# Performance work log

Measured on AMD Instinct MI355X. Metric: run time of the kernel, lower is better.

## Reference

```python
import jax, jax.numpy as jnp
import numpy as np

B, N, H = 8192, 8, 256
EDGE_DIM = 16
HALF = EDGE_DIM // 2  # 8: emb half + scalar half
THR = 0.4
PAIR_OFFS = [(0, N), (0, 2 * N), (N, 2 * N)]  # (text,audio), (text,facial), (audio,facial)
E_PER = 6 * (N - 1) + 6 * N  # 90 edges per sample


def _base_edge_index():
    # Static per-sample topology (matches the torch loop ordering exactly).
    src, dst = [], []
    for m in range(3):  # temporal edges, both directions interleaved
        for i in range(N - 1):
            u, v = m * N + i, m * N + i + 1
            src += [u, v]; dst += [v, u]
    for oa, ob in PAIR_OFFS:  # cross-modal edges
        for i in range(N):
            src += [oa + i, ob + i]; dst += [ob + i, oa + i]
    return np.array([src, dst], dtype=np.int64)  # (2, E_PER)

_BASE_EI = _base_edge_index()


def _l2norm(x):
    return x / jnp.maximum(jnp.linalg.norm(x, axis=-1, keepdims=True), 1e-12)


def setup_inputs() -> dict:
    key = jax.random.key(0)
    ks = jax.random.split(key, 6)
    s = 1.0 / np.sqrt(H)
    return {
        "z_text_segs": jax.random.normal(ks[0], (B, N, H), jnp.float32),
        "z_audio_segs": jax.random.normal(ks[1], (B, N, H), jnp.float32),
        "z_facial_segs": jax.random.normal(ks[2], (B, N, H), jnp.float32),
        "Wq": jax.random.normal(ks[3], (H // 2, H), jnp.float32) * s,
        "bq": jnp.zeros((H // 2,), jnp.float32),
        "Wk": jax.random.normal(ks[4], (H // 2, H), jnp.float32) * s,
        "bk": jnp.zeros((H // 2,), jnp.float32),
        "emb": jax.random.normal(ks[5], (5, HALF), jnp.float32),
    }


def reference(z_text_segs, z_audio_segs, z_facial_segs, Wq, bq, Wk, bk, emb):
    nodes = jnp.concatenate([z_text_segs, z_audio_segs, z_facial_segs], axis=1)  # (B, 3N, H)
    q = _l2norm(nodes @ Wq.T + bq)  # (B, 3N, H/2)
    k = _l2norm(nodes @ Wk.T + bk)

    # Cross-modal discrepancy, pair-major then segment (matches loop order): P = 3N
    a_idx = np.concatenate([oa + np.arange(N) for oa, _ in PAIR_OFFS])
    b_idx = np.concatenate([ob + np.arange(N) for _, ob in PAIR_OFFS])
    disc = 1.0 - jax.nn.sigmoid(jnp.einsum('bph,bph->bp', q[:, a_idx], k[:, b_idx]))  # (B, P)

    etype = jnp.where(disc > THR, 4, 3)  # (B, P) int
    z = jnp.zeros_like(disc)
    # scalar half: [disc_w, temp_dist, direction, etype/4, pad...]
    cross_scal = jnp.stack([disc, z, z, etype.astype(jnp.float32) / 4.0] + [z] * (HALF - 4), axis=-1)
    cross_attr = jnp.concatenate([emb[etype], cross_scal], axis=-1)  # (B, P, EDGE_DIM)
    cross_attr = jnp.repeat(cross_attr, 2, axis=1)  # both directions share the attr

    # Temporal edge attrs: constant per modality m in {0,1,2}
    mz = jnp.zeros((3,), jnp.float32)
    t_scal = jnp.stack([mz, jnp.full((3,), 1.0 / N), jnp.ones((3,)),
                        jnp.arange(3, dtype=jnp.float32) / 4.0] + [mz] * (HALF - 4), axis=-1)
    t_attr = jnp.concatenate([emb[:3], t_scal], axis=-1)  # (3, EDGE_DIM)
    t_attr = jnp.repeat(t_attr, 2 * (N - 1), axis=0)  # (6(N-1), EDGE_DIM)
    t_attr = jnp.broadcast_to(t_attr, (B,) + t_attr.shape)

    edge_attr = jnp.concatenate([t_attr, cross_attr], axis=1).reshape(B * E_PER, EDGE_DIM)

    ei = _BASE_EI[:, None, :] + (np.arange(B, dtype=np.int64) * 3 * N)[None, :, None]
    edge_index = jnp.asarray(ei.reshape(2, B * E_PER))

    node_feats = nodes.reshape(B * 3 * N, H)
    batch_vec = jnp.repeat(jnp.arange(B), 3 * N)
    return node_feats, edge_index, edge_attr, batch_vec
```

## Files before the change

### kernel.cpp

```cpp
#include <hip/hip_runtime.h>
#include <stdint.h>

#define BB 8192
#define HH 256
#define HO 128
#define NODES 24
#define EPER 90
#define NF_SIZE (BB * NODES * HH)
#define EI_OFF  NF_SIZE
#define EI_SIZE (2 * BB * EPER)
#define EA_OFF  (EI_OFF + EI_SIZE)
#define EA_SIZE (BB * EPER * 16)
#define BV_OFF  (EA_OFF + EA_SIZE)

typedef float f4 __attribute__((ext_vector_type(4)));

#define SL(dst, base, IMM) \
    asm volatile("s_load_dwordx4 %0, %1, " IMM : "=s"(dst) : "s"(base))

#define SWAIT8(a0,a1,a2,a3,a4,a5,a6,a7) \
    asm volatile("s_waitcnt lgkmcnt(0)" \
                 : "+s"(a0),"+s"(a1),"+s"(a2),"+s"(a3), \
                   "+s"(a4),"+s"(a5),"+s"(a6),"+s"(a7))

#define FMA4(acc, W_, X_) \
    acc = fmaf((W_)[0],(X_)[0],acc); acc = fmaf((W_)[1],(X_)[1],acc); \
    acc = fmaf((W_)[2],(X_)[2],acc); acc = fmaf((W_)[3],(X_)[3],acc);

#define LD8(BUF, ADDR) \
    SL(BUF##0, ADDR, "0x0");    SL(BUF##1, ADDR, "0x400"); \
    SL(BUF##2, ADDR, "0x800");  SL(BUF##3, ADDR, "0xc00"); \
    SL(BUF##4, ADDR, "0x1000"); SL(BUF##5, ADDR, "0x1400"); \
    SL(BUF##6, ADDR, "0x1800"); SL(BUF##7, ADDR, "0x1c00");

#define C8(ACC0, ACC1, BUF) \
    FMA4(ACC0[0], w0, BUF##0) FMA4(ACC1[0], w1, BUF##0) \
    FMA4(ACC0[1], w0, BUF##1) FMA4(ACC1[1], w1, BUF##1) \
    FMA4(ACC0[2], w0, BUF##2) FMA4(ACC1[2], w1, BUF##2) \
    FMA4(ACC0[3], w0, BUF##3) FMA4(ACC1[3], w1, BUF##3) \
    FMA4(ACC0[4], w0, BUF##4) FMA4(ACC1[4], w1, BUF##4) \
    FMA4(ACC0[5], w0, BUF##5) FMA4(ACC1[5], w1, BUF##5) \
    FMA4(ACC0[6], w0, BUF##6) FMA4(ACC1[6], w1, BUF##6) \
    FMA4(ACC0[7], w0, BUF##7) FMA4(ACC1[7], w1, BUF##7)

__global__ __launch_bounds__(256) void transpose_w(
    const float4* __restrict__ Wq4, const float4* __restrict__ Wk4,
    float4* __restrict__ ws)
{
    int idx = blockIdx.x * 256 + threadIdx.x;
    const float4* src = (idx < 8192) ? Wq4 : Wk4;
    int j  = idx & 8191;
    int o  = j >> 6;
    int kk = j & 63;
    float4 v = src[j];
    ws[(idx & 8192) + kk * 128 + o] = v;
}

__global__ __launch_bounds__(256) void htdg_kernel(
    const float* __restrict__ zt, const float* __restrict__ za,
    const float* __restrict__ zf,
    const float* __restrict__ bq, const float* __restrict__ bk,
    const float* __restrict__ emb, const float* __restrict__ wt,
    float* __restrict__ out)
{
    __shared__ float uv[2 * 32 * HO];
    __shared__ float nrm_part[2][256];
    __shared__ float dot_part[2][192];
    __shared__ float rnorm_s[2][32];
    __shared__ float disc_s[2][24];
    __shared__ int   et_s[2][24];
    __shared__ float emb_s[40];

    const int b0  = blockIdx.x * 2;
    const int tid = threadIdx.x;

    {
        const f4* zt4 = (const f4*)zt + (size_t)b0 * 512;
        const f4* za4 = (const f4*)za + (size_t)b0 * 512;
        const f4* zf4 = (const f4*)zf + (size_t)b0 * 512;
        f4* nf = (f4*)out + (size_t)b0 * 1536;
        #pragma unroll
        for (int it = 0; it < 12; ++it) {
            int j = tid + it * 256;
            int s = (it >= 6);
            int rem = j - s * 1536;
            int m = rem >> 9, w = rem & 511;
            const f4* sp = (m == 0 ? zt4 : m == 1 ? za4 : zf4) + s * 512 + w;
            nf[j] = *sp;
        }
        if (tid < 40) emb_s[tid] = emb[tid];
    }

    #pragma unroll
    for (int s = 0; s < 2; ++s) {
        int b = b0 + s;
        int j = tid;
        if (j < 180) {
            int d = (j >= 90) ? 1 : 0;
            int e = j - d * 90;
            int ss, dd;
            if (e < 42) {
                int m = e / 14;
                int r = e - m * 14;
                int i = r >> 1;
                int u = m * 8 + i;
                if (r & 1) { ss = u + 1; dd = u; } else { ss = u; dd = u + 1; }
            } else {
                int p  = (e - 42) >> 1;
                int pr = p >> 3;
                int i  = p & 7;
                int a  = (pr == 2 ? 8 : 0) + i;
                int bb = (pr == 0 ? 8 : 16) + i;
                if (e & 1) { ss = bb; dd = a; } else { ss = a; dd = bb; }
            }
            int val = ((d == 0) ? ss : dd) + b * 24;
            out[(size_t)EI_OFF + (size_t)d * (BB * EPER) + (size_t)b * EPER + e] = (float)val;
        }
        if (tid < 24) out[(size_t)BV_OFF + (size_t)b * 24 + tid] = (float)b;
    }

    {
        const int wave = tid >> 6;
        const int lane = tid & 63;
        const f4* Wt4 = (const f4*)wt + ((wave < 2) ? 0 : 8192);
        const float* zsel = (wave == 0) ? zt : (wave == 3) ? zf : za;
        const float* bias = (wave < 2) ? bq : bk;
        const int slotBase = wave * 8;

        uint64_t xb;
        {
            uint64_t v = (uint64_t)zsel + (uint64_t)b0 * 8192;
            uint32_t lo = __builtin_amdgcn_readfirstlane((uint32_t)v);
            uint32_t hi = __builtin_amdgcn_readfirstlane((uint32_t)(v >> 32));
            xb = ((uint64_t)hi << 32) | lo;
        }

        float A0r0[8] = {0,0,0,0,0,0,0,0}, A0r1[8] = {0,0,0,0,0,0,0,0};
        float A1r0[8] = {0,0,0,0,0,0,0,0}, A1r1[8] = {0,0,0,0,0,0,0,0};
        f4 x0, x1, x2, x3, x4, x5, x6, x7;
        f4 y0, y1, y2, y3, y4, y5, y6, y7;

        f4 w0 = Wt4[lane];
        f4 w1 = Wt4[64 + lane];

        LD8(x, xb);

        for (int kk = 0; kk < 64; ++kk) {
            int kn = (kk < 63) ? kk + 1 : 63;
            f4 nw0 = Wt4[kn * 128 + lane];
            f4 nw1 = Wt4[kn * 128 + 64 + lane];
            uint64_t aB = xb + (uint64_t)(8192 + kk * 16);
            uint64_t aA = xb + (uint64_t)(kn * 16);

            SWAIT8(x0, x1, x2, x3, x4, x5, x6, x7);
            LD8(y, aB);
            C8(A0r0, A0r1, x);

            SWAIT8(y0, y1, y2, y3, y4, y5, y6, y7);
            LD8(x, aA);
            C8(A1r0, A1r1, y);

            w0 = nw0; w1 = nw1;
        }
        asm volatile("s_waitcnt lgkmcnt(0)");

        float bb0 = bias[lane], bb1 = bias[lane + 64];
        #pragma unroll
        for (int n = 0; n < 8; ++n) {
            uv[(slotBase + n) * HO + lane]             = A0r0[n] + bb0;
            uv[(slotBase + n) * HO + 64 + lane]        = A0r1[n] + bb1;
            uv[4096 + (slotBase + n) * HO + lane]      = A1r0[n] + bb0;
            uv[4096 + (slotBase + n) * HO + 64 + lane] = A1r1[n] + bb1;
        }
    }
    __syncthreads();

    #pragma unroll
    for (int s = 0; s < 2; ++s) {
        const float* uvS = uv + s * 4096;
        {
            int slot = tid >> 3, part = tid & 7;
            const float* u = &uvS[slot * HO + part * 16];
            float sum = 0.f;
            #pragma unroll
            for (int o = 0; o < 16; ++o) { float v = u[o]; sum += v * v; }
            nrm_part[s][tid] = sum;
        }
        if (tid < 192) {
            int p = tid >> 3, part = tid & 7;
            int pr = p >> 3, i = p & 7;
            int aslot = (pr == 2 ? 8 : 0) + i;
            int bslot = (pr == 0 ? 16 : 24) + i;
            const float* ua = &uvS[aslot * HO + part * 16];
            const float* vb = &uvS[bslot * HO + part * 16];
            float sum = 0.f;
            #pragma unroll
            for (int o = 0; o < 16; ++o) sum += ua[o] * vb[o];
            dot_part[s][tid] = sum;
        }
    }
    __syncthreads();
    if (tid < 64) {
        int s = tid >> 5, sl = tid & 31;
        float sum = 0.f;
        #pragma unroll
        for (int j = 0; j < 8; ++j) sum += nrm_part[s][sl * 8 + j];
        rnorm_s[s][sl] = 1.0f / fmaxf(sqrtf(sum), 1e-12f);
    }
    __syncthreads();
    if (tid < 64) {
        int s = tid >> 5, p = tid & 31;
        if (p < 24) {
            float sum = 0.f;
            #pragma unroll
            for (int j = 0; j < 8; ++j) sum += dot_part[s][p * 8 + j];
            int pr = p >> 3, i = p & 7;
            int aslot = (pr == 2 ? 8 : 0) + i;
            int bslot = (pr == 0 ? 16 : 24) + i;
            float t   = sum * rnorm_s[s][aslot] * rnorm_s[s][bslot];
            float dsc = 1.0f / (1.0f + expf(t));
            disc_s[s][p] = dsc;
            et_s[s][p]   = (dsc > 0.4f) ? 4 : 3;
        }
    }
    __syncthreads();

    #pragma unroll
    for (int s = 0; s < 2; ++s) {
        float* ea = out + (size_t)EA_OFF + (size_t)(b0 + s) * (EPER * 16);
        #pragma unroll
        for (int it = 0; it < 6; ++it) {
            int j = tid + it * 256;
            if (j < 1440) {
                int row = j >> 4, c = j & 15;
                float val;
                if (row < 42) {
                    int m = row / 14;
                    if      (c < 8)   val = emb_s[m * 8 + c];
                    else if (c == 9)  val = 0.125f;
                    else if (c == 10) val = 1.0f;
                    else if (c == 11) val = (float)m * 0.25f;
                    else              val = 0.0f;
                } else {
                    int p  = (row - 42) >> 1;
                    int et = et_s[s][p];
                    if      (c < 8)   val = emb_s[et * 8 + c];
                    else if (c == 8)  val = disc_s[s][p];
                    else if (c == 11) val = (float)et * 0.25f;
                    else              val = 0.0f;
                }
                ea[j] = val;
            }
        }
    }
}

extern "C" void kernel_launch(void* const* d_in, const int* in_sizes, int n_in,
                              void* d_out, int out_size, void* d_ws, size_t ws_size,
                              hipStream_t stream) {
    const float* zt  = (const float*)d_in[0];
    const float* za  = (const float*)d_in[1];
    const float* zf  = (const float*)d_in[2];
    const float* Wq  = (const float*)d_in[3];
    const float* bq  = (const float*)d_in[4];
    const float* Wk  = (const float*)d_in[5];
    const float* bk  = (const float*)d_in[6];
    const float* emb = (const float*)d_in[7];

    float4* ws = (float4*)d_ws;
    transpose_w<<<64, 256, 0, stream>>>((const float4*)Wq, (const float4*)Wk, ws);
    htdg_kernel<<<BB / 2, 256, 0, stream>>>(zt, za, zf, bq, bk, emb,
                                            (const float*)ws, (float*)d_out);
}
```

Measured before the change: 659.6 us.

## Compute norms and discrepancy dots in registers via wave shuffles, stage only keys in LDS

The q/k projections now stay in registers. Norms are reduced with cross-lane xor shuffles inside each wave, and only the key vectors plus their reciprocal norms go to shared memory. The query waves then compute the cross-modal dot products directly against the staged keys. This removes the full uv staging buffer, the partial-sum arrays and two block barriers, and shrinks LDS use. It adds many serial shuffle reductions, leaves the wave-0 path with double work, and sets a launch-bounds occupancy hint of 8 that may constrain registers.

```diff
diff --git a/kernel.cpp b/kernel.cpp
--- a/kernel.cpp
+++ b/kernel.cpp
@@ -4,9 +4,8 @@
 #define BB 8192
 #define HH 256
 #define HO 128
-#define NODES 24
 #define EPER 90
-#define NF_SIZE (BB * NODES * HH)
+#define NF_SIZE (BB * 24 * HH)
 #define EI_OFF  NF_SIZE
 #define EI_SIZE (2 * BB * EPER)
 #define EA_OFF  (EI_OFF + EI_SIZE)
@@ -56,23 +55,23 @@
     ws[(idx & 8192) + kk * 128 + o] = v;
 }
 
-__global__ __launch_bounds__(256) void htdg_kernel(
+__global__ __launch_bounds__(256, 8) void htdg_kernel(
     const float* __restrict__ zt, const float* __restrict__ za,
     const float* __restrict__ zf,
     const float* __restrict__ bq, const float* __restrict__ bk,
     const float* __restrict__ emb, const float* __restrict__ wt,
     float* __restrict__ out)
 {
-    __shared__ float uv[2 * 32 * HO];
-    __shared__ float nrm_part[2][256];
-    __shared__ float dot_part[2][192];
-    __shared__ float rnorm_s[2][32];
+    __shared__ float kbuf[2 * 16 * HO];
+    __shared__ float rnorm_k[2][16];
     __shared__ float disc_s[2][24];
     __shared__ int   et_s[2][24];
     __shared__ float emb_s[40];
 
     const int b0  = blockIdx.x * 2;
     const int tid = threadIdx.x;
+    const int wave = tid >> 6;
+    const int lane = tid & 63;
 
     {
         const f4* zt4 = (const f4*)zt + (size_t)b0 * 512;
@@ -119,13 +118,11 @@
         if (tid < 24) out[(size_t)BV_OFF + (size_t)b * 24 + tid] = (float)b;
     }
 
+    float q0[8], q1[8], q2[8], q3[8];
     {
-        const int wave = tid >> 6;
-        const int lane = tid & 63;
         const f4* Wt4 = (const f4*)wt + ((wave < 2) ? 0 : 8192);
         const float* zsel = (wave == 0) ? zt : (wave == 3) ? zf : za;
         const float* bias = (wave < 2) ? bq : bk;
-        const int slotBase = wave * 8;
 
         uint64_t xb;
         {
@@ -167,60 +164,71 @@
         float bb0 = bias[lane], bb1 = bias[lane + 64];
         #pragma unroll
         for (int n = 0; n < 8; ++n) {
-            uv[(slotBase + n) * HO + lane]             = A0r0[n] + bb0;
-            uv[(slotBase + n) * HO + 64 + lane]        = A0r1[n] + bb1;
-            uv[4096 + (slotBase + n) * HO + lane]      = A1r0[n] + bb0;
-            uv[4096 + (slotBase + n) * HO + 64 + lane] = A1r1[n] + bb1;
+            q0[n] = A0r0[n] + bb0;
+            q1[n] = A0r1[n] + bb1;
+            q2[n] = A1r0[n] + bb0;
+            q3[n] = A1r1[n] + bb1;
+        }
+    }
+
+    if (wave >= 2) {
+        int sb = (wave - 2) * 8;
+        #pragma unroll
+        for (int n = 0; n < 8; ++n) {
+            kbuf[(sb + n) * HO + lane]            = q0[n];
+            kbuf[(sb + n) * HO + 64 + lane]       = q1[n];
+            kbuf[(16 + sb + n) * HO + lane]       = q2[n];
+            kbuf[(16 + sb + n) * HO + 64 + lane]  = q3[n];
+        }
+    }
+    float rn0[8], rn1[8];
+    #pragma unroll
+    for (int n = 0; n < 8; ++n) {
+        float p0 = q0[n] * q0[n] + q1[n] * q1[n];
+        float p1 = q2[n] * q2[n] + q3[n] * q3[n];
+        #pragma unroll
+        for (int m = 1; m < 64; m <<= 1) {
+            p0 += __shfl_xor(p0, m, 64);
+            p1 += __shfl_xor(p1, m, 64);
+        }
+        rn0[n] = 1.0f / fmaxf(sqrtf(p0), 1e-12f);
+        rn1[n] = 1.0f / fmaxf(sqrtf(p1), 1e-12f);
+    }
+    if (wave >= 2 && lane == 0) {
+        int sb = (wave - 2) * 8;
+        #pragma unroll
+        for (int n = 0; n < 8; ++n) {
+            rnorm_k[0][sb + n] = rn0[n];
+            rnorm_k[1][sb + n] = rn1[n];
         }
     }
     __syncthreads();
 
-    #pragma unroll
-    for (int s = 0; s < 2; ++s) {
-        const float* uvS = uv + s * 4096;
-        {
-            int slot = tid >> 3, part = tid & 7;
-            const float* u = &uvS[slot * HO + part * 16];
-            float sum = 0.f;
+    if (wave < 2) {
+        #pragma unroll
+        for (int i = 0; i < 8; ++i) {
+            const int reps = (wave == 0) ? 2 : 1;
             #pragma unroll
-            for (int o = 0; o < 16; ++o) { float v = u[o]; sum += v * v; }
-            nrm_part[s][tid] = sum;
-        }
-        if (tid < 192) {
-            int p = tid >> 3, part = tid & 7;
-            int pr = p >> 3, i = p & 7;
-            int aslot = (pr == 2 ? 8 : 0) + i;
-            int bslot = (pr == 0 ? 16 : 24) + i;
-            const float* ua = &uvS[aslot * HO + part * 16];
-            const float* vb = &uvS[bslot * HO + part * 16];
-            float sum = 0.f;
-            #pragma unroll
-            for (int o = 0; o < 16; ++o) sum += ua[o] * vb[o];
-            dot_part[s][tid] = sum;
-        }
-    }
-    __syncthreads();
-    if (tid < 64) {
-        int s = tid >> 5, sl = tid & 31;
-        float sum = 0.f;
-        #pragma unroll
-        for (int j = 0; j < 8; ++j) sum += nrm_part[s][sl * 8 + j];
-        rnorm_s[s][sl] = 1.0f / fmaxf(sqrtf(sum), 1e-12f);
-    }
-    __syncthreads();
-    if (tid < 64) {
-        int s = tid >> 5, p = tid & 31;
-        if (p < 24) {
-            float sum = 0.f;
-            #pragma unroll
-            for (int j = 0; j < 8; ++j) sum += dot_part[s][p * 8 + j];
-            int pr = p >> 3, i = p & 7;
-            int aslot = (pr == 2 ? 8 : 0) + i;
-            int bslot = (pr == 0 ? 16 : 24) + i;
-            float t   = sum * rnorm_s[s][aslot] * rnorm_s[s][bslot];
-            float dsc = 1.0f / (1.0f + expf(t));
-            disc_s[s][p] = dsc;
-            et_s[s][p]   = (dsc > 0.4f) ? 4 : 3;
+            for (int rep = 0; rep < reps; ++rep) {
+                int b16 = (wave == 0 && rep == 0) ? i : (8 + i);
+                int p   = (wave == 0) ? ((rep == 0) ? i : 8 + i) : (16 + i);
+                #pragma unroll
+                for (int s = 0; s < 2; ++s) {
+                    const float* kp = &kbuf[(s * 16 + b16) * HO];
+                    float ka = kp[lane], kc = kp[64 + lane];
+                    float part = (s ? q2[i] : q0[i]) * ka
+                               + (s ? q3[i] : q1[i]) * kc;
+                    #pragma unroll
+                    for (int m = 1; m < 64; m <<= 1)
+                        part += __shfl_xor(part, m, 64);
+                    float t   = part * (s ? rn1[i] : rn0[i]) * rnorm_k[s][b16];
+                    float dsc = 1.0f / (1.0f + expf(t));
+                    if (lane == 0) {
+                        disc_s[s][p] = dsc;
+                        et_s[s][p]   = (dsc > 0.4f) ? 4 : 3;
+                    }
+                }
+            }
         }
     }
     __syncthreads();
```

New measurement: 725.1 us. 9.9% more time.
